# Kernel optimization log

Measured on AMD Instinct MI355X. Metric: run time of the kernel, lower is better.

Reference implementation:

```python
import jax, jax.numpy as jnp
import numpy as np

GT_MASK_LEN = 128   # processor_dct.gt_mask_len
N_KEEP = 256        # processor_dct.n_keep


def _zigzag_flat_positions(n):
    """Row-major flat index of the k-th element in JPEG zigzag order of an n x n grid."""
    order = []
    for s in range(2 * n - 1):
        if s % 2 == 0:  # even diagonals traverse up-right
            for i in range(min(s, n - 1), max(-1, s - n), -1):
                order.append((i, s - i))
        else:
            for j in range(min(s, n - 1), max(-1, s - n), -1):
                order.append((s - j, j))
    return np.array([i * n + j for (i, j) in order], dtype=np.int64)


def _dct_matrix(n):
    """Orthonormal DCT-II matrix C (cv2.dct). cv2.idct(Y) == C.T @ Y @ C in 2-D."""
    k = np.arange(n)[:, None].astype(np.float64)
    m = np.arange(n)[None, :].astype(np.float64)
    C = np.sqrt(2.0 / n) * np.cos(np.pi * (2 * m + 1) * k / (2 * n))
    C[0, :] = np.sqrt(1.0 / n)
    return C.astype(np.float32)

_ZZ_POS = jnp.asarray(_zigzag_flat_positions(GT_MASK_LEN)[:N_KEEP])
_DCT_C = jnp.asarray(_dct_matrix(GT_MASK_LEN))


def setup_inputs() -> dict:
    key = jax.random.key(0)
    k1, k2, k3, k4 = jax.random.split(key, 4)
    B, R, C = 8, 300, 91
    pred_logits = jax.random.normal(k1, (B, R, C), dtype=jnp.float32)
    pred_boxes = jax.random.uniform(k2, (B, R, 4), dtype=jnp.float32) * 0.5 + 0.25
    pred_vectors = jax.random.normal(k3, (B, R, N_KEEP), dtype=jnp.float32)
    target_sizes = jax.random.randint(k4, (B, 2), 512, 1334, dtype=jnp.int32)
    return {"pred_logits": pred_logits, "pred_boxes": pred_boxes,
            "pred_vectors": pred_vectors, "target_sizes": target_sizes}


def reference(pred_logits, pred_boxes, pred_vectors, target_sizes):
    L = GT_MASK_LEN
    # --- classification scores ---
    prob = jax.nn.sigmoid(pred_logits)            # [B,R,C]
    scores = prob.max(axis=2)                     # [B,R]
    labels = prob.argmax(axis=2)                  # [B,R] int
    # --- boxes: cxcywh -> xyxy, rescale to image size ---
    cx, cy, w, h = jnp.split(pred_boxes, 4, axis=-1)
    boxes = jnp.concatenate([cx - 0.5 * w, cy - 0.5 * h,
                             cx + 0.5 * w, cy + 0.5 * h], axis=-1)  # [B,R,4]
    ts = target_sizes.astype(jnp.float32)
    img_h, img_w = ts[:, 0], ts[:, 1]
    scale_fct = jnp.stack([img_w, img_h, img_w, img_h], axis=1)     # [B,4]
    boxes = boxes * scale_fct[:, None, :]
    # --- masks: inverse zigzag scatter + batched separable 2-D IDCT ---
    B, R, _ = pred_vectors.shape
    flat = jnp.zeros((B, R, L * L), dtype=pred_vectors.dtype)
    flat = flat.at[:, :, _ZZ_POS].set(pred_vectors)
    coef = flat.reshape(B, R, L, L)
    # cv2.idct(Y) = C^T Y C (orthonormal DCT-III)
    re_mask = jnp.einsum('iu,bruv,vj->brij', _DCT_C.T, coef, _DCT_C)  # [B,R,L,L]
    max_v = re_mask.max(axis=(-2, -1), keepdims=True)
    min_v = re_mask.min(axis=(-2, -1), keepdims=True)
    masks = jnp.where(re_mask > (max_v + min_v) * 0.5, 1.0, 0.0).astype(jnp.float32)
    return scores, labels, boxes, masks
```

## Files before the change

### kernel.cpp

```cpp
#include <hip/hip_runtime.h>
#include <math.h>

#define NROWS 2400
#define NCLS  91
#define L     128
#define KSUB  23
#define NKEEP 256

__global__ void __launch_bounds__(256)
build_csub_kernel(float* __restrict__ csub)
{
    __shared__ double tab[512];
    const int tid = threadIdx.x;
    for (int t = tid; t < 512; t += 256)
        tab[t] = cos((3.14159265358979323846 / 256.0) * (double)t);
    __syncthreads();
    const double s0 = sqrt(1.0 / 128.0);
    for (int idx = tid; idx < KSUB * L; idx += 256) {
        const int u = idx >> 7, m = idx & 127;
        float v;
        if (u == 0) v = (float)s0;
        else        v = (float)(0.125 * tab[((2 * m + 1) * u) & 511]);
        csub[idx] = v;
    }
}

#define COEF_OFF 5888
#define RED_OFF  6440
#define SMEM_FLOATS 6448

__global__ void __launch_bounds__(256)
postproc_kernel(const float* __restrict__ logits,
                const float* __restrict__ pboxes,
                const float* __restrict__ vecs,
                const int*   __restrict__ tsz,
                const float* __restrict__ csub_g,
                float* __restrict__ out)
{
    __shared__ float smem[SMEM_FLOATS];
    const int br  = blockIdx.x;
    const int tid = threadIdx.x;

    if (tid < 64) {
        const float* lrow = logits + (size_t)br * NCLS;
        float p = 1.0f / (1.0f + expf(-lrow[tid]));
        int   bi = tid;
        if (tid < NCLS - 64) {
            float p2 = 1.0f / (1.0f + expf(-lrow[tid + 64]));
            if (p2 > p) { p = p2; bi = tid + 64; }
        }
        #pragma unroll
        for (int off = 32; off > 0; off >>= 1) {
            float po = __shfl_xor(p, off, 64);
            int   io = __shfl_xor(bi, off, 64);
            if (po > p || (po == p && io < bi)) { p = po; bi = io; }
        }
        if (tid == 0) {
            out[br] = p;
            out[NROWS + br] = (float)bi;
            const int b = br / 300;
            const float W = (float)tsz[2 * b + 1];
            const float H = (float)tsz[2 * b + 0];
            const float4 bx = *(const float4*)(pboxes + (size_t)br * 4);
            float4 o;
            o.x = (bx.x - 0.5f * bx.z) * W;
            o.y = (bx.y - 0.5f * bx.w) * H;
            o.z = (bx.x + 0.5f * bx.z) * W;
            o.w = (bx.y + 0.5f * bx.w) * H;
            *(float4*)(out + 2 * NROWS + (size_t)br * 4) = o;
        }
    }

    for (int t = tid; t < 736; t += 256)
        ((float4*)smem)[t] = ((const float4*)csub_g)[t];

    float* coef = &smem[COEF_OFF];
    for (int t = tid; t < KSUB * 24; t += 256) {
        const int u = t / 24, v = t - u * 24;
        const int s = u + v;
        if (v == 23 || s > 22 || (s == 22 && u < 20)) coef[t] = 0.0f;
    }
    {
        const int k = tid;
        int s = 0;
        while ((s + 1) * (s + 2) / 2 <= k) ++s;
        const int r = k - s * (s + 1) / 2;
        const int u  = (s & 1) ? r : (s - r);
        const int vv = (s & 1) ? (s - r) : r;
        coef[u * 24 + vv] = vecs[(size_t)br * NKEEP + k];
    }
    __syncthreads();

    float* M1 = &smem[2944];
    {
        const int i = tid & 127;
        float cs[KSUB];
        #pragma unroll
        for (int u = 0; u < KSUB; ++u) cs[u] = smem[u * L + i];
        if (tid < 128) {
            #pragma unroll
            for (int v = 0; v < 12; ++v) {
                float a = 0.0f;
                #pragma unroll
                for (int u = 0; u < KSUB; ++u) a += cs[u] * coef[u * 24 + v];
                M1[v * L + i] = a;
            }
        } else {
            #pragma unroll
            for (int v = 12; v < KSUB; ++v) {
                float a = 0.0f;
                #pragma unroll
                for (int u = 0; u < KSUB; ++u) a += cs[u] * coef[u * 24 + v];
                M1[v * L + i] = a;
            }
        }
    }
    __syncthreads();

    const int tx = tid & 31, ty = tid >> 5;
    const int j0 = tx << 2, i0 = ty << 4;
    float acc[16][4];
    #pragma unroll
    for (int r = 0; r < 16; ++r)
        #pragma unroll
        for (int q = 0; q < 4; ++q) acc[r][q] = 0.0f;

    for (int v = 0; v < KSUB; ++v) {
        const float4 c  = *(const float4*)&smem[v * L + j0];
        const float4 m0 = *(const float4*)&M1[v * L + i0];
        const float4 m1 = *(const float4*)&M1[v * L + i0 + 4];
        const float4 m2 = *(const float4*)&M1[v * L + i0 + 8];
        const float4 m3 = *(const float4*)&M1[v * L + i0 + 12];
        const float mv[16] = { m0.x, m0.y, m0.z, m0.w,
                               m1.x, m1.y, m1.z, m1.w,
                               m2.x, m2.y, m2.z, m2.w,
                               m3.x, m3.y, m3.z, m3.w };
        #pragma unroll
        for (int r = 0; r < 16; ++r) {
            acc[r][0] += mv[r] * c.x;
            acc[r][1] += mv[r] * c.y;
            acc[r][2] += mv[r] * c.z;
            acc[r][3] += mv[r] * c.w;
        }
    }

    float mn = acc[0][0], mx = acc[0][0];
    #pragma unroll
    for (int r = 0; r < 16; ++r)
        #pragma unroll
        for (int q = 0; q < 4; ++q) {
            mn = fminf(mn, acc[r][q]);
            mx = fmaxf(mx, acc[r][q]);
        }
    #pragma unroll
    for (int off = 32; off > 0; off >>= 1) {
        mn = fminf(mn, __shfl_xor(mn, off, 64));
        mx = fmaxf(mx, __shfl_xor(mx, off, 64));
    }
    const int w = tid >> 6;
    if ((tid & 63) == 0) { smem[RED_OFF + w] = mn; smem[RED_OFF + 4 + w] = mx; }
    __syncthreads();
    const float gmn = fminf(fminf(smem[RED_OFF + 0], smem[RED_OFF + 1]),
                            fminf(smem[RED_OFF + 2], smem[RED_OFF + 3]));
    const float gmx = fmaxf(fmaxf(smem[RED_OFF + 4], smem[RED_OFF + 5]),
                            fmaxf(smem[RED_OFF + 6], smem[RED_OFF + 7]));
    const float thr = (gmx + gmn) * 0.5f;

    float* omask = out + 6 * NROWS + (size_t)br * (L * L);
    #pragma unroll
    for (int r = 0; r < 16; ++r) {
        float4 o;
        o.x = acc[r][0] > thr ? 1.0f : 0.0f;
        o.y = acc[r][1] > thr ? 1.0f : 0.0f;
        o.z = acc[r][2] > thr ? 1.0f : 0.0f;
        o.w = acc[r][3] > thr ? 1.0f : 0.0f;
        *(float4*)&omask[(i0 + r) * L + j0] = o;
    }
}

extern "C" void kernel_launch(void* const* d_in, const int* in_sizes, int n_in,
                              void* d_out, int out_size, void* d_ws, size_t ws_size,
                              hipStream_t stream)
{
    const float* logits = (const float*)d_in[0];
    const float* pboxes = (const float*)d_in[1];
    const float* vecs   = (const float*)d_in[2];
    const int*   tsz    = (const int*)d_in[3];
    float* out  = (float*)d_out;
    float* csub = (float*)d_ws;
    (void)in_sizes; (void)n_in; (void)out_size; (void)ws_size;

    build_csub_kernel<<<dim3(1), dim3(256), 0, stream>>>(csub);
    postproc_kernel<<<dim3(NROWS), dim3(256), 0, stream>>>(logits, pboxes, vecs, tsz, csub, out);
}
```

Baseline: 197.7 us.

## Move score and box work into setup kernel and slim mask kernel

Classification argmax and box rescaling move out of the per-row mask kernel into the setup kernel, which now runs 10 blocks with one thread per row instead of a single block. The mask kernel gains a launch_bounds occupancy hint, loads the M1 vectors one float4 group at a time to reduce register pressure, and writes mask output with nontemporal stores. The aim is higher occupancy and lower write-cache pollution in the dominant mask kernel, at the cost of a serial 91-class loop per thread in the setup kernel.

```diff
diff --git a/kernel.cpp b/kernel.cpp
--- a/kernel.cpp
+++ b/kernel.cpp
@@ -7,21 +7,54 @@
 #define KSUB  23
 #define NKEEP 256
 
+typedef float vfloat4 __attribute__((ext_vector_type(4)));
+
 __global__ void __launch_bounds__(256)
-build_csub_kernel(float* __restrict__ csub)
+setup_kernel(const float* __restrict__ logits,
+             const float* __restrict__ pboxes,
+             const int*   __restrict__ tsz,
+             float* __restrict__ csub,
+             float* __restrict__ out)
 {
-    __shared__ double tab[512];
     const int tid = threadIdx.x;
-    for (int t = tid; t < 512; t += 256)
-        tab[t] = cos((3.14159265358979323846 / 256.0) * (double)t);
-    __syncthreads();
-    const double s0 = sqrt(1.0 / 128.0);
-    for (int idx = tid; idx < KSUB * L; idx += 256) {
-        const int u = idx >> 7, m = idx & 127;
-        float v;
-        if (u == 0) v = (float)s0;
-        else        v = (float)(0.125 * tab[((2 * m + 1) * u) & 511]);
-        csub[idx] = v;
+
+    if (blockIdx.x == 0) {
+        __shared__ double tab[512];
+        for (int t = tid; t < 512; t += 256)
+            tab[t] = cos((3.14159265358979323846 / 256.0) * (double)t);
+        __syncthreads();
+        const double s0 = sqrt(1.0 / 128.0);
+        for (int idx = tid; idx < KSUB * L; idx += 256) {
+            const int u = idx >> 7, m = idx & 127;
+            float v;
+            if (u == 0) v = (float)s0;
+            else        v = (float)(0.125 * tab[((2 * m + 1) * u) & 511]);
+            csub[idx] = v;
+        }
+    }
+
+    const int row = blockIdx.x * 256 + tid;
+    if (row < NROWS) {
+        const float* lrow = logits + (size_t)row * NCLS;
+        float best = 1.0f / (1.0f + expf(-lrow[0]));
+        int   bi = 0;
+        for (int c = 1; c < NCLS; ++c) {
+            const float p = 1.0f / (1.0f + expf(-lrow[c]));
+            if (p > best) { best = p; bi = c; }
+        }
+        out[row] = best;
+        out[NROWS + row] = (float)bi;
+
+        const int b = row / 300;
+        const float W = (float)tsz[2 * b + 1];
+        const float H = (float)tsz[2 * b + 0];
+        const float4 bx = *(const float4*)(pboxes + (size_t)row * 4);
+        float4 o;
+        o.x = (bx.x - 0.5f * bx.z) * W;
+        o.y = (bx.y - 0.5f * bx.w) * H;
+        o.z = (bx.x + 0.5f * bx.z) * W;
+        o.w = (bx.y + 0.5f * bx.w) * H;
+        *(float4*)(out + 2 * NROWS + (size_t)row * 4) = o;
     }
 }
 
@@ -29,47 +62,14 @@
 #define RED_OFF  6440
 #define SMEM_FLOATS 6448
 
-__global__ void __launch_bounds__(256)
-postproc_kernel(const float* __restrict__ logits,
-                const float* __restrict__ pboxes,
-                const float* __restrict__ vecs,
-                const int*   __restrict__ tsz,
-                const float* __restrict__ csub_g,
-                float* __restrict__ out)
+__global__ void __launch_bounds__(256, 4)
+mask_kernel(const float* __restrict__ vecs,
+            const float* __restrict__ csub_g,
+            float* __restrict__ out)
 {
     __shared__ float smem[SMEM_FLOATS];
     const int br  = blockIdx.x;
     const int tid = threadIdx.x;
-
-    if (tid < 64) {
-        const float* lrow = logits + (size_t)br * NCLS;
-        float p = 1.0f / (1.0f + expf(-lrow[tid]));
-        int   bi = tid;
-        if (tid < NCLS - 64) {
-            float p2 = 1.0f / (1.0f + expf(-lrow[tid + 64]));
-            if (p2 > p) { p = p2; bi = tid + 64; }
-        }
-        #pragma unroll
-        for (int off = 32; off > 0; off >>= 1) {
-            float po = __shfl_xor(p, off, 64);
-            int   io = __shfl_xor(bi, off, 64);
-            if (po > p || (po == p && io < bi)) { p = po; bi = io; }
-        }
-        if (tid == 0) {
-            out[br] = p;
-            out[NROWS + br] = (float)bi;
-            const int b = br / 300;
-            const float W = (float)tsz[2 * b + 1];
-            const float H = (float)tsz[2 * b + 0];
-            const float4 bx = *(const float4*)(pboxes + (size_t)br * 4);
-            float4 o;
-            o.x = (bx.x - 0.5f * bx.z) * W;
-            o.y = (bx.y - 0.5f * bx.w) * H;
-            o.z = (bx.x + 0.5f * bx.z) * W;
-            o.w = (bx.y + 0.5f * bx.w) * H;
-            *(float4*)(out + 2 * NROWS + (size_t)br * 4) = o;
-        }
-    }
 
     for (int t = tid; t < 736; t += 256)
         ((float4*)smem)[t] = ((const float4*)csub_g)[t];
@@ -126,21 +126,18 @@
         for (int q = 0; q < 4; ++q) acc[r][q] = 0.0f;
 
     for (int v = 0; v < KSUB; ++v) {
-        const float4 c  = *(const float4*)&smem[v * L + j0];
-        const float4 m0 = *(const float4*)&M1[v * L + i0];
-        const float4 m1 = *(const float4*)&M1[v * L + i0 + 4];
-        const float4 m2 = *(const float4*)&M1[v * L + i0 + 8];
-        const float4 m3 = *(const float4*)&M1[v * L + i0 + 12];
-        const float mv[16] = { m0.x, m0.y, m0.z, m0.w,
-                               m1.x, m1.y, m1.z, m1.w,
-                               m2.x, m2.y, m2.z, m2.w,
-                               m3.x, m3.y, m3.z, m3.w };
+        const float4 c = *(const float4*)&smem[v * L + j0];
         #pragma unroll
-        for (int r = 0; r < 16; ++r) {
-            acc[r][0] += mv[r] * c.x;
-            acc[r][1] += mv[r] * c.y;
-            acc[r][2] += mv[r] * c.z;
-            acc[r][3] += mv[r] * c.w;
+        for (int g = 0; g < 4; ++g) {
+            const float4 m = *(const float4*)&M1[v * L + i0 + 4 * g];
+            acc[4*g+0][0] += m.x * c.x; acc[4*g+0][1] += m.x * c.y;
+            acc[4*g+0][2] += m.x * c.z; acc[4*g+0][3] += m.x * c.w;
+            acc[4*g+1][0] += m.y * c.x; acc[4*g+1][1] += m.y * c.y;
+            acc[4*g+1][2] += m.y * c.z; acc[4*g+1][3] += m.y * c.w;
+            acc[4*g+2][0] += m.z * c.x; acc[4*g+2][1] += m.z * c.y;
+            acc[4*g+2][2] += m.z * c.z; acc[4*g+2][3] += m.z * c.w;
+            acc[4*g+3][0] += m.w * c.x; acc[4*g+3][1] += m.w * c.y;
+            acc[4*g+3][2] += m.w * c.z; acc[4*g+3][3] += m.w * c.w;
         }
     }
 
@@ -169,12 +166,12 @@
     float* omask = out + 6 * NROWS + (size_t)br * (L * L);
     #pragma unroll
     for (int r = 0; r < 16; ++r) {
-        float4 o;
+        vfloat4 o;
         o.x = acc[r][0] > thr ? 1.0f : 0.0f;
         o.y = acc[r][1] > thr ? 1.0f : 0.0f;
         o.z = acc[r][2] > thr ? 1.0f : 0.0f;
         o.w = acc[r][3] > thr ? 1.0f : 0.0f;
-        *(float4*)&omask[(i0 + r) * L + j0] = o;
+        __builtin_nontemporal_store(o, (vfloat4*)&omask[(i0 + r) * L + j0]);
     }
 }
 
@@ -190,6 +187,6 @@
     float* csub = (float*)d_ws;
     (void)in_sizes; (void)n_in; (void)out_size; (void)ws_size;
 
-    build_csub_kernel<<<dim3(1), dim3(256), 0, stream>>>(csub);
-    postproc_kernel<<<dim3(NROWS), dim3(256), 0, stream>>>(logits, pboxes, vecs, tsz, csub, out);
+    setup_kernel<<<dim3(10),    dim3(256), 0, stream>>>(logits, pboxes, tsz, csub, out);
+    mask_kernel <<<dim3(NROWS), dim3(256), 0, stream>>>(vecs, csub, out);
 }
```

After: 232.3 us. 1.17x slower.

## Fold DCT basis construction into main kernel and vectorize coefficient loads

Applied to the files above, without the earlier changes.

Removes the separate single-block kernel that built the truncated DCT basis in workspace; each block now computes the cosine table in double precision into shared memory (reusing the M1 region) and derives the basis itself. This drops one kernel launch and its serialization, but makes every one of the 2400 blocks do 512 double-precision cosines plus an extra barrier. The first-stage product is rewritten to load coefficients as float4 with register accumulators, and the second-stage loop is restructured to load M1 per group.

```diff
diff --git a/kernel.cpp b/kernel.cpp
--- a/kernel.cpp
+++ b/kernel.cpp
@@ -7,24 +7,8 @@
 #define KSUB  23
 #define NKEEP 256
 
-__global__ void __launch_bounds__(256)
-build_csub_kernel(float* __restrict__ csub)
-{
-    __shared__ double tab[512];
-    const int tid = threadIdx.x;
-    for (int t = tid; t < 512; t += 256)
-        tab[t] = cos((3.14159265358979323846 / 256.0) * (double)t);
-    __syncthreads();
-    const double s0 = sqrt(1.0 / 128.0);
-    for (int idx = tid; idx < KSUB * L; idx += 256) {
-        const int u = idx >> 7, m = idx & 127;
-        float v;
-        if (u == 0) v = (float)s0;
-        else        v = (float)(0.125 * tab[((2 * m + 1) * u) & 511]);
-        csub[idx] = v;
-    }
-}
-
+#define TAB_OFF  2944
+#define M1_OFF   2944
 #define COEF_OFF 5888
 #define RED_OFF  6440
 #define SMEM_FLOATS 6448
@@ -34,7 +18,6 @@
                 const float* __restrict__ pboxes,
                 const float* __restrict__ vecs,
                 const int*   __restrict__ tsz,
-                const float* __restrict__ csub_g,
                 float* __restrict__ out)
 {
     __shared__ float smem[SMEM_FLOATS];
@@ -71,9 +54,21 @@
         }
     }
 
-    for (int t = tid; t < 736; t += 256)
-        ((float4*)smem)[t] = ((const float4*)csub_g)[t];
-
+    double* tab = (double*)&smem[TAB_OFF];
+    for (int t = tid; t < 512; t += 256)
+        tab[t] = cos((3.14159265358979323846 / 256.0) * (double)t);
+    __syncthreads();
+
+    {
+        const double s0 = sqrt(1.0 / 128.0);
+        for (int idx = tid; idx < KSUB * L; idx += 256) {
+            const int u = idx >> 7, m = idx & 127;
+            float v;
+            if (u == 0) v = (float)s0;
+            else        v = (float)(0.125 * tab[((2 * m + 1) * u) & 511]);
+            smem[idx] = v;
+        }
+    }
     float* coef = &smem[COEF_OFF];
     for (int t = tid; t < KSUB * 24; t += 256) {
         const int u = t / 24, v = t - u * 24;
@@ -91,28 +86,45 @@
     }
     __syncthreads();
 
-    float* M1 = &smem[2944];
+    float* M1 = &smem[M1_OFF];
     {
         const int i = tid & 127;
         float cs[KSUB];
         #pragma unroll
         for (int u = 0; u < KSUB; ++u) cs[u] = smem[u * L + i];
+
         if (tid < 128) {
-            #pragma unroll
-            for (int v = 0; v < 12; ++v) {
-                float a = 0.0f;
-                #pragma unroll
-                for (int u = 0; u < KSUB; ++u) a += cs[u] * coef[u * 24 + v];
-                M1[v * L + i] = a;
+            float a[12];
+            #pragma unroll
+            for (int v = 0; v < 12; ++v) a[v] = 0.0f;
+            #pragma unroll
+            for (int u = 0; u < KSUB; ++u) {
+                const float4 c0 = *(const float4*)&coef[u * 24 + 0];
+                const float4 c1 = *(const float4*)&coef[u * 24 + 4];
+                const float4 c2 = *(const float4*)&coef[u * 24 + 8];
+                const float cu = cs[u];
+                a[0]  += cu * c0.x; a[1]  += cu * c0.y; a[2]  += cu * c0.z; a[3]  += cu * c0.w;
+                a[4]  += cu * c1.x; a[5]  += cu * c1.y; a[6]  += cu * c1.z; a[7]  += cu * c1.w;
+                a[8]  += cu * c2.x; a[9]  += cu * c2.y; a[10] += cu * c2.z; a[11] += cu * c2.w;
             }
+            #pragma unroll
+            for (int v = 0; v < 12; ++v) M1[v * L + i] = a[v];
         } else {
-            #pragma unroll
-            for (int v = 12; v < KSUB; ++v) {
-                float a = 0.0f;
-                #pragma unroll
-                for (int u = 0; u < KSUB; ++u) a += cs[u] * coef[u * 24 + v];
-                M1[v * L + i] = a;
+            float a[11];
+            #pragma unroll
+            for (int v = 0; v < 11; ++v) a[v] = 0.0f;
+            #pragma unroll
+            for (int u = 0; u < KSUB; ++u) {
+                const float4 c0 = *(const float4*)&coef[u * 24 + 12];
+                const float4 c1 = *(const float4*)&coef[u * 24 + 16];
+                const float4 c2 = *(const float4*)&coef[u * 24 + 20];
+                const float cu = cs[u];
+                a[0] += cu * c0.x; a[1] += cu * c0.y; a[2]  += cu * c0.z; a[3] += cu * c0.w;
+                a[4] += cu * c1.x; a[5] += cu * c1.y; a[6]  += cu * c1.z; a[7] += cu * c1.w;
+                a[8] += cu * c2.x; a[9] += cu * c2.y; a[10] += cu * c2.z;
             }
+            #pragma unroll
+            for (int v = 0; v < 11; ++v) M1[(v + 12) * L + i] = a[v];
         }
     }
     __syncthreads();
@@ -126,21 +138,18 @@
         for (int q = 0; q < 4; ++q) acc[r][q] = 0.0f;
 
     for (int v = 0; v < KSUB; ++v) {
-        const float4 c  = *(const float4*)&smem[v * L + j0];
-        const float4 m0 = *(const float4*)&M1[v * L + i0];
-        const float4 m1 = *(const float4*)&M1[v * L + i0 + 4];
-        const float4 m2 = *(const float4*)&M1[v * L + i0 + 8];
-        const float4 m3 = *(const float4*)&M1[v * L + i0 + 12];
-        const float mv[16] = { m0.x, m0.y, m0.z, m0.w,
-                               m1.x, m1.y, m1.z, m1.w,
-                               m2.x, m2.y, m2.z, m2.w,
-                               m3.x, m3.y, m3.z, m3.w };
-        #pragma unroll
-        for (int r = 0; r < 16; ++r) {
-            acc[r][0] += mv[r] * c.x;
-            acc[r][1] += mv[r] * c.y;
-            acc[r][2] += mv[r] * c.z;
-            acc[r][3] += mv[r] * c.w;
+        const float4 c = *(const float4*)&smem[v * L + j0];
+        #pragma unroll
+        for (int g = 0; g < 4; ++g) {
+            const float4 m = *(const float4*)&M1[v * L + i0 + 4 * g];
+            acc[4*g+0][0] += m.x * c.x; acc[4*g+0][1] += m.x * c.y;
+            acc[4*g+0][2] += m.x * c.z; acc[4*g+0][3] += m.x * c.w;
+            acc[4*g+1][0] += m.y * c.x; acc[4*g+1][1] += m.y * c.y;
+            acc[4*g+1][2] += m.y * c.z; acc[4*g+1][3] += m.y * c.w;
+            acc[4*g+2][0] += m.z * c.x; acc[4*g+2][1] += m.z * c.y;
+            acc[4*g+2][2] += m.z * c.z; acc[4*g+2][3] += m.z * c.w;
+            acc[4*g+3][0] += m.w * c.x; acc[4*g+3][1] += m.w * c.y;
+            acc[4*g+3][2] += m.w * c.z; acc[4*g+3][3] += m.w * c.w;
         }
     }
 
@@ -186,10 +195,8 @@
     const float* pboxes = (const float*)d_in[1];
     const float* vecs   = (const float*)d_in[2];
     const int*   tsz    = (const int*)d_in[3];
-    float* out  = (float*)d_out;
-    float* csub = (float*)d_ws;
-    (void)in_sizes; (void)n_in; (void)out_size; (void)ws_size;
-
-    build_csub_kernel<<<dim3(1), dim3(256), 0, stream>>>(csub);
-    postproc_kernel<<<dim3(NROWS), dim3(256), 0, stream>>>(logits, pboxes, vecs, tsz, csub, out);
+    float* out = (float*)d_out;
+    (void)d_ws; (void)ws_size; (void)in_sizes; (void)n_in; (void)out_size;
+
+    postproc_kernel<<<dim3(NROWS), dim3(256), 0, stream>>>(logits, pboxes, vecs, tsz, out);
 }
```

Result: faster. 191.0 us (-3.4%).
